# Kernel optimization log

Measured on AMD Instinct MI355X. Metric: run time of the kernel, lower is better.

The kernel has to match this reference:

```python
import jax, jax.numpy as jnp
import numpy as np

B, S, D, H, DK = 2, 2048, 1024, 16, 64
NEG = -1000000000.0


def setup_inputs() -> dict:
    key = jax.random.key(0)
    ks = jax.random.split(key, 7)
    scale = 1.0 / np.sqrt(D)
    return {
        "pos_encode_toks": jax.random.normal(ks[0], (B, S, D), dtype=jnp.float32),
        "Wq": jax.random.uniform(ks[1], (D, D), minval=-scale, maxval=scale, dtype=jnp.float32),
        "bq": jax.random.uniform(ks[2], (D,), minval=-scale, maxval=scale, dtype=jnp.float32),
        "Wk": jax.random.uniform(ks[3], (D, D), minval=-scale, maxval=scale, dtype=jnp.float32),
        "bk": jax.random.uniform(ks[4], (D,), minval=-scale, maxval=scale, dtype=jnp.float32),
        "W0": jax.random.uniform(ks[5], (D, D), minval=-scale, maxval=scale, dtype=jnp.float32),
        "b0": jax.random.uniform(ks[6], (D,), minval=-scale, maxval=scale, dtype=jnp.float32),
    }


def reference(pos_encode_toks, Wq, bq, Wk, bk, W0, b0):
    x = pos_encode_toks
    b, s, d = x.shape
    # NOTE: the original module computes V with Wq (a bug in the source) -- replicated here.
    q = (x @ Wq + bq).reshape(b, s, H, DK).transpose(0, 2, 1, 3)  # [B,H,S,DK]
    k = (x @ Wk + bk).reshape(b, s, H, DK).transpose(0, 2, 1, 3)
    v = q  # V = Wq(x), same projection as Q
    scores = jnp.einsum("bhqd,bhkd->bhqk", q, k) / np.sqrt(DK)
    causal = jnp.tril(jnp.ones((s, s), dtype=bool))
    scores = jnp.where(causal, scores, NEG)
    att_pat = jax.nn.softmax(scores, axis=-1)
    att = jnp.einsum("bhqk,bhkd->bhqd", att_pat, v)
    att = att.transpose(0, 2, 1, 3).reshape(b, s, d)
    return att @ W0 + b0
```

## Files before the change

### kernel.cpp

```cpp
#include <hip/hip_runtime.h>
#include <cstdint>
#include <cstddef>


#define AS1 __attribute__((address_space(1)))
#define AS3 __attribute__((address_space(3)))

typedef unsigned short u16;
typedef __attribute__((ext_vector_type(8))) short bf16x8;
typedef __attribute__((ext_vector_type(4))) float f32x4;

__device__ __forceinline__ u16 f2bf(float f) {
  uint32_t u = __builtin_bit_cast(uint32_t, f);
  u += 0x7fffu + ((u >> 16) & 1u);
  return (u16)(u >> 16);
}

__device__ __forceinline__ void gload16(const void* g, void* l) {
  __builtin_amdgcn_global_load_lds((const AS1 uint32_t*)(uintptr_t)g,
                                   (AS3 uint32_t*)(uintptr_t)l, 16, 0, 0);
}

__global__ __launch_bounds__(256) void cvt_x_kernel(const float* __restrict__ x,
                                                    u16* __restrict__ xb) {
  const int stride = gridDim.x * blockDim.x;
  int i = blockIdx.x * blockDim.x + threadIdx.x;
  const float4* x4 = (const float4*)x;
  ushort4* o4 = (ushort4*)xb;
  for (; i < 1048576; i += stride) {
    float4 v = x4[i];
    ushort4 o;
    o.x = f2bf(v.x); o.y = f2bf(v.y); o.z = f2bf(v.z); o.w = f2bf(v.w);
    o4[i] = o;
  }
}

__global__ __launch_bounds__(256) void transpose_w_kernel(
    const float* __restrict__ Wq, const float* __restrict__ Wk,
    const float* __restrict__ W0, u16* __restrict__ wqT,
    u16* __restrict__ wkT, u16* __restrict__ w0T) {
  const float* src; u16* dst;
  if (blockIdx.z == 0)      { src = Wq; dst = wqT; }
  else if (blockIdx.z == 1) { src = Wk; dst = wkT; }
  else                      { src = W0; dst = w0T; }
  __shared__ u16 T[64][65];
  const int k0 = blockIdx.y * 64, n0 = blockIdx.x * 64;
  const int c = threadIdx.x & 63, r0 = threadIdx.x >> 6;
#pragma unroll
  for (int i = 0; i < 16; ++i) {
    int r = i * 4 + r0;
    T[r][c] = f2bf(src[(size_t)(k0 + r) * 1024 + n0 + c]);
  }
  __syncthreads();
#pragma unroll
  for (int i = 0; i < 16; ++i) {
    int r = i * 4 + r0;
    dst[(size_t)(n0 + r) * 1024 + k0 + c] = T[c][r];
  }
}

__global__ __launch_bounds__(256) void transpose_q_kernel(const u16* __restrict__ q,
                                                          u16* __restrict__ qT) {
  const int bh = blockIdx.y;
  const int s0 = blockIdx.x * 64;
  const u16* src = q + (size_t)bh * 2048 * 64;
  u16* dst = qT + (size_t)bh * 64 * 2048;
  __shared__ u16 T[64][65];
  const int c = threadIdx.x & 63, r0 = threadIdx.x >> 6;
#pragma unroll
  for (int i = 0; i < 16; ++i) {
    int r = i * 4 + r0;
    T[r][c] = src[(size_t)(s0 + r) * 64 + c];
  }
  __syncthreads();
#pragma unroll
  for (int i = 0; i < 16; ++i) {
    int r = i * 4 + r0;
    dst[(size_t)r * 2048 + s0 + c] = T[c][r];
  }
}

template <int EPI>
__global__ __launch_bounds__(256) void gemm_kernel(
    const u16* __restrict__ A, const u16* __restrict__ BT,
    const float* __restrict__ bias, u16* __restrict__ Ob,
    float* __restrict__ Of) {
  __shared__ __align__(16) u16 As[64][64];
  __shared__ __align__(16) u16 Bs[128][64];
  const int tid = threadIdx.x, wid = tid >> 6, lane = tid & 63;
  const int l15 = lane & 15, lg = lane >> 4;
  const int bid = blockIdx.y * gridDim.x + blockIdx.x;
  const int swb = (bid & 7) * 64 + (bid >> 3);
  const int m0 = (((swb >> 6) * 8) + ((swb >> 3) & 7)) * 64;
  const int n0 = (swb & 7) * 128;
  const int wr = (wid >> 1) * 32, wc = (wid & 1) * 64;
  const int srow = lane >> 3;
  const int gz = (((lane & 7) ^ srow) * 8);

  f32x4 acc[2][4] = {};

  for (int k0 = 0; k0 < 1024; k0 += 64) {
#pragma unroll
    for (int i = 0; i < 2; ++i) {
      int chunk = wid * 2 + i;
      gload16(&A[(size_t)(m0 + chunk * 8 + srow) * 1024 + k0 + gz], &As[chunk * 8][0]);
    }
#pragma unroll
    for (int i = 0; i < 4; ++i) {
      int chunk = wid * 4 + i;
      gload16(&BT[(size_t)(n0 + chunk * 8 + srow) * 1024 + k0 + gz], &Bs[chunk * 8][0]);
    }
    __syncthreads();
#pragma unroll
    for (int kf = 0; kf < 2; ++kf) {
      const int cg = ((kf * 4 + lg) ^ (lane & 7)) * 8;
      bf16x8 af[2], bfr[4];
#pragma unroll
      for (int m = 0; m < 2; ++m)
        af[m] = *(const bf16x8*)&As[wr + m * 16 + l15][cg];
#pragma unroll
      for (int n = 0; n < 4; ++n)
        bfr[n] = *(const bf16x8*)&Bs[wc + n * 16 + l15][cg];
#pragma unroll
      for (int m = 0; m < 2; ++m)
#pragma unroll
        for (int n = 0; n < 4; ++n)
          acc[m][n] = __builtin_amdgcn_mfma_f32_16x16x32_bf16(af[m], bfr[n], acc[m][n], 0, 0, 0);
    }
    __syncthreads();
  }

  float bv[4];
#pragma unroll
  for (int n = 0; n < 4; ++n) bv[n] = bias[n0 + wc + n * 16 + l15];
#pragma unroll
  for (int m = 0; m < 2; ++m) {
#pragma unroll
    for (int r = 0; r < 4; ++r) {
      const int gm = m0 + wr + m * 16 + lg * 4 + r;
#pragma unroll
      for (int n = 0; n < 4; ++n) {
        const int gn = n0 + wc + n * 16 + l15;
        float v = acc[m][n][r] + bv[n];
        if constexpr (EPI == 2) {
          Of[(size_t)gm * 1024 + gn] = v;
        } else {
          const int b = gm >> 11, s = gm & 2047;
          const int h = gn >> 6, dk = gn & 63;
          Ob[(((size_t)(b * 16 + h)) * 2048 + s) * 64 + dk] = f2bf(v);
        }
      }
    }
  }
}

__global__ __launch_bounds__(256) void attn_kernel(const u16* __restrict__ Q,
                                                   const u16* __restrict__ K,
                                                   const u16* __restrict__ QT,
                                                   u16* __restrict__ ATT) {
  __shared__ __align__(16) u16 Ks[64][64];
  __shared__ __align__(16) u16 Vs[64][64];
  __shared__ __align__(16) u16 Ps[4][16][64];
  const int tid = threadIdx.x, wid = tid >> 6, lane = tid & 63;
  const int l15 = lane & 15, lg = lane >> 4;
  const int bid = blockIdx.y * 16 + blockIdx.x;
  const int swb = (bid & 7) * 64 + (bid >> 3);
  const int bh = (swb >> 6) * 4 + ((swb >> 4) & 3);
  const int qx = swb & 15;
  const size_t base = (size_t)bh * 2048 * 64;
  const int bb = bh >> 4, hh = bh & 15;
  const int srow = lane >> 3;
  const int gz = (((lane & 7) ^ srow) * 8);

  for (int half = 0; half < 2; ++half) {
    const int qt = half ? (31 - qx) : qx;
    const int q0 = qt * 64;
    const int wrow = q0 + wid * 16;

    bf16x8 qf[2];
#pragma unroll
    for (int kf = 0; kf < 2; ++kf)
      qf[kf] = *(const bf16x8*)&Q[base + (size_t)(wrow + l15) * 64 + kf * 32 + lg * 8];

    f32x4 o[4] = {};
    float mx[4], sm[4];
#pragma unroll
    for (int r = 0; r < 4; ++r) { mx[r] = -3e38f; sm[r] = 0.f; }

    for (int t = 0; t <= qt; ++t) {
      const int kv0 = t * 64;
#pragma unroll
      for (int i = 0; i < 2; ++i) {
        int chunk = wid * 2 + i;
        gload16(&K[base + (size_t)(kv0 + chunk * 8 + srow) * 64 + gz], &Ks[chunk * 8][0]);
        gload16(&QT[base + (size_t)(chunk * 8 + srow) * 2048 + kv0 + gz], &Vs[chunk * 8][0]);
      }
      __syncthreads();

      f32x4 sc[4] = {};
#pragma unroll
      for (int kf = 0; kf < 2; ++kf) {
        const int cg = ((kf * 4 + lg) ^ (lane & 7)) * 8;
        bf16x8 kb[4];
#pragma unroll
        for (int n = 0; n < 4; ++n)
          kb[n] = *(const bf16x8*)&Ks[n * 16 + l15][cg];
        __builtin_amdgcn_s_setprio(1);
#pragma unroll
        for (int n = 0; n < 4; ++n)
          sc[n] = __builtin_amdgcn_mfma_f32_16x16x32_bf16(qf[kf], kb[n], sc[n], 0, 0, 0);
        __builtin_amdgcn_s_setprio(0);
      }

      const bool maskt = (t == qt);
      float pr[4][4], rmax[4];
#pragma unroll
      for (int r = 0; r < 4; ++r) rmax[r] = -3e38f;
#pragma unroll
      for (int n = 0; n < 4; ++n)
#pragma unroll
        for (int r = 0; r < 4; ++r) {
          float v = sc[n][r] * 0.125f;
          if (maskt && (n * 16 + l15 > wid * 16 + lg * 4 + r)) v = -1e30f;
          pr[n][r] = v;
          rmax[r] = fmaxf(rmax[r], v);
        }
#pragma unroll
      for (int r = 0; r < 4; ++r)
#pragma unroll
        for (int d = 1; d < 16; d <<= 1)
          rmax[r] = fmaxf(rmax[r], __shfl_xor(rmax[r], d));

      float alpha[4];
#pragma unroll
      for (int r = 0; r < 4; ++r) {
        float mnew = fmaxf(mx[r], rmax[r]);
        alpha[r] = __expf(mx[r] - mnew);
        mx[r] = mnew;
        float rs = 0.f;
#pragma unroll
        for (int n = 0; n < 4; ++n) {
          float p = __expf(pr[n][r] - mnew);
          pr[n][r] = p;
          rs += p;
        }
        sm[r] = sm[r] * alpha[r] + rs;
      }
#pragma unroll
      for (int n = 0; n < 4; ++n)
#pragma unroll
        for (int r = 0; r < 4; ++r) o[n][r] *= alpha[r];

#pragma unroll
      for (int n = 0; n < 4; ++n)
#pragma unroll
        for (int r = 0; r < 4; ++r) {
          const int prow = lg * 4 + r;
          const int pcol = (n * 16 + l15) ^ ((prow & 7) << 3);
          Ps[wid][prow][pcol] = f2bf(pr[n][r]);
        }
      asm volatile("s_waitcnt lgkmcnt(0)" ::: "memory");

#pragma unroll
      for (int kf = 0; kf < 2; ++kf) {
        const int cg = ((kf * 4 + lg) ^ (lane & 7)) * 8;
        bf16x8 pa = *(const bf16x8*)&Ps[wid][l15][cg];
        bf16x8 vb[4];
#pragma unroll
        for (int n = 0; n < 4; ++n)
          vb[n] = *(const bf16x8*)&Vs[n * 16 + l15][cg];
        __builtin_amdgcn_s_setprio(1);
#pragma unroll
        for (int n = 0; n < 4; ++n)
          o[n] = __builtin_amdgcn_mfma_f32_16x16x32_bf16(pa, vb[n], o[n], 0, 0, 0);
        __builtin_amdgcn_s_setprio(0);
      }
      __syncthreads();
    }

#pragma unroll
    for (int r = 0; r < 4; ++r)
#pragma unroll
      for (int d = 1; d < 16; d <<= 1) sm[r] += __shfl_xor(sm[r], d);

#pragma unroll
    for (int r = 0; r < 4; ++r) {
      const float inv = 1.0f / sm[r];
      const int s = wrow + lg * 4 + r;
#pragma unroll
      for (int n = 0; n < 4; ++n)
        ATT[((size_t)(bb * 2048 + s)) * 1024 + hh * 64 + n * 16 + l15] =
            f2bf(o[n][r] * inv);
    }
  }
}

extern "C" void kernel_launch(void* const* d_in, const int* in_sizes, int n_in,
                              void* d_out, int out_size, void* d_ws, size_t ws_size,
                              hipStream_t stream) {
  const float* x  = (const float*)d_in[0];
  const float* Wq = (const float*)d_in[1];
  const float* bq = (const float*)d_in[2];
  const float* Wk = (const float*)d_in[3];
  const float* bk = (const float*)d_in[4];
  const float* W0 = (const float*)d_in[5];
  const float* b0 = (const float*)d_in[6];
  float* out = (float*)d_out;

  char* ws = (char*)d_ws;
  u16* xb  = (u16*)(ws + 0);
  u16* wqT = (u16*)(ws + 8388608);
  u16* wkT = (u16*)(ws + 10485760);
  u16* w0T = (u16*)(ws + 12582912);
  u16* q   = (u16*)(ws + 14680064);
  u16* k   = (u16*)(ws + 23068672);
  u16* qT  = (u16*)(ws + 31457280);
  u16* att = (u16*)(ws + 39845888);

  cvt_x_kernel<<<dim3(1024), dim3(256), 0, stream>>>(x, xb);
  transpose_w_kernel<<<dim3(16, 16, 3), dim3(256), 0, stream>>>(Wq, Wk, W0, wqT, wkT, w0T);
  gemm_kernel<0><<<dim3(64, 8), dim3(256), 0, stream>>>(xb, wqT, bq, q, nullptr);
  gemm_kernel<0><<<dim3(64, 8), dim3(256), 0, stream>>>(xb, wkT, bk, k, nullptr);
  transpose_q_kernel<<<dim3(32, 32), dim3(256), 0, stream>>>(q, qT);
  attn_kernel<<<dim3(16, 32), dim3(256), 0, stream>>>(q, k, qT, att);
  gemm_kernel<2><<<dim3(64, 8), dim3(256), 0, stream>>>(att, w0T, b0, nullptr, out);
}
```

Baseline: 200.0 us.

## Fuse Q/K projections, enlarge GEMM tiles, double-buffer attention with lazy rescaling

The Q and K projection GEMMs are merged into one launch over the concatenated, already contiguous Wq/Wk transposes, with per-column bias and output selection. The GEMM moves to 128x128 tiles with 512 threads. The attention kernel now gives each block a single query tile, longest first, and double-buffers K/V loads in shared memory so the next tile's loads overlap compute. Softmax uses exp2 with the scale folded in, and rescales the running max only when it grows by more than 8. This adds LDS use and register pressure per block, and the larger GEMM tiles give fewer blocks for the output projection.

```diff
diff --git a/kernel.cpp b/kernel.cpp
--- a/kernel.cpp
+++ b/kernel.cpp
@@ -1,4 +1,5 @@
 #include <hip/hip_runtime.h>
+#include <hip/hip_bf16.h>
 #include <cstdint>
 #include <cstddef>
 
@@ -80,218 +81,242 @@
   }
 }
 
-template <int EPI>
-__global__ __launch_bounds__(256) void gemm_kernel(
+template <int EPI, int NTILES>
+__global__ __launch_bounds__(512, 4) void gemm_kernel(
     const u16* __restrict__ A, const u16* __restrict__ BT,
-    const float* __restrict__ bias, u16* __restrict__ Ob,
-    float* __restrict__ Of) {
-  __shared__ __align__(16) u16 As[64][64];
+    const float* __restrict__ bias0, const float* __restrict__ bias1,
+    u16* __restrict__ Oq, u16* __restrict__ Ok, float* __restrict__ Of) {
+  __shared__ __align__(16) u16 As[128][64];
   __shared__ __align__(16) u16 Bs[128][64];
   const int tid = threadIdx.x, wid = tid >> 6, lane = tid & 63;
   const int l15 = lane & 15, lg = lane >> 4;
-  const int bid = blockIdx.y * gridDim.x + blockIdx.x;
-  const int swb = (bid & 7) * 64 + (bid >> 3);
-  const int m0 = (((swb >> 6) * 8) + ((swb >> 3) & 7)) * 64;
-  const int n0 = (swb & 7) * 128;
-  const int wr = (wid >> 1) * 32, wc = (wid & 1) * 64;
+  constexpr int NH = NTILES / 2;
+  const int bid = blockIdx.x;
+  const int c = bid & 7, l = bid >> 3;
+  const int m0 = ((c >> 1) * 8 + l / NH) * 128;
+  const int n0 = ((c & 1) * NH + l % NH) * 128;
+  const int wrow = (wid >> 2) * 64, wcol = (wid & 3) * 32;
   const int srow = lane >> 3;
-  const int gz = (((lane & 7) ^ srow) * 8);
-
-  f32x4 acc[2][4] = {};
+  const int gz = ((lane & 7) ^ srow) * 8;
+
+  f32x4 acc[4][2] = {};
 
   for (int k0 = 0; k0 < 1024; k0 += 64) {
 #pragma unroll
     for (int i = 0; i < 2; ++i) {
-      int chunk = wid * 2 + i;
-      gload16(&A[(size_t)(m0 + chunk * 8 + srow) * 1024 + k0 + gz], &As[chunk * 8][0]);
-    }
-#pragma unroll
-    for (int i = 0; i < 4; ++i) {
-      int chunk = wid * 4 + i;
-      gload16(&BT[(size_t)(n0 + chunk * 8 + srow) * 1024 + k0 + gz], &Bs[chunk * 8][0]);
+      int ch = wid * 2 + i;
+      gload16(&A[(size_t)(m0 + ch * 8 + srow) * 1024 + k0 + gz], &As[ch * 8][0]);
+      gload16(&BT[(size_t)(n0 + ch * 8 + srow) * 1024 + k0 + gz], &Bs[ch * 8][0]);
     }
     __syncthreads();
 #pragma unroll
     for (int kf = 0; kf < 2; ++kf) {
       const int cg = ((kf * 4 + lg) ^ (lane & 7)) * 8;
-      bf16x8 af[2], bfr[4];
-#pragma unroll
-      for (int m = 0; m < 2; ++m)
-        af[m] = *(const bf16x8*)&As[wr + m * 16 + l15][cg];
-#pragma unroll
-      for (int n = 0; n < 4; ++n)
-        bfr[n] = *(const bf16x8*)&Bs[wc + n * 16 + l15][cg];
-#pragma unroll
-      for (int m = 0; m < 2; ++m)
-#pragma unroll
-        for (int n = 0; n < 4; ++n)
+      bf16x8 af[4], bfr[2];
+#pragma unroll
+      for (int m = 0; m < 4; ++m)
+        af[m] = *(const bf16x8*)&As[wrow + m * 16 + l15][cg];
+#pragma unroll
+      for (int n = 0; n < 2; ++n)
+        bfr[n] = *(const bf16x8*)&Bs[wcol + n * 16 + l15][cg];
+#pragma unroll
+      for (int m = 0; m < 4; ++m)
+#pragma unroll
+        for (int n = 0; n < 2; ++n)
           acc[m][n] = __builtin_amdgcn_mfma_f32_16x16x32_bf16(af[m], bfr[n], acc[m][n], 0, 0, 0);
     }
     __syncthreads();
   }
 
-  float bv[4];
-#pragma unroll
-  for (int n = 0; n < 4; ++n) bv[n] = bias[n0 + wc + n * 16 + l15];
-#pragma unroll
-  for (int m = 0; m < 2; ++m) {
+  float bv[2];
+#pragma unroll
+  for (int n = 0; n < 2; ++n) {
+    const int gn = n0 + wcol + n * 16 + l15;
+    if constexpr (EPI == 0)
+      bv[n] = (gn < 1024) ? bias0[gn] : bias1[gn - 1024];
+    else
+      bv[n] = bias0[gn];
+  }
+#pragma unroll
+  for (int m = 0; m < 4; ++m) {
 #pragma unroll
     for (int r = 0; r < 4; ++r) {
-      const int gm = m0 + wr + m * 16 + lg * 4 + r;
-#pragma unroll
-      for (int n = 0; n < 4; ++n) {
-        const int gn = n0 + wc + n * 16 + l15;
+      const int gm = m0 + wrow + m * 16 + lg * 4 + r;
+#pragma unroll
+      for (int n = 0; n < 2; ++n) {
+        const int gn = n0 + wcol + n * 16 + l15;
         float v = acc[m][n][r] + bv[n];
         if constexpr (EPI == 2) {
           Of[(size_t)gm * 1024 + gn] = v;
         } else {
+          u16* dst = (gn < 1024) ? Oq : Ok;
+          const int gg = gn & 1023;
           const int b = gm >> 11, s = gm & 2047;
-          const int h = gn >> 6, dk = gn & 63;
-          Ob[(((size_t)(b * 16 + h)) * 2048 + s) * 64 + dk] = f2bf(v);
+          const int h = gg >> 6, dk = gg & 63;
+          dst[(((size_t)(b * 16 + h)) * 2048 + s) * 64 + dk] = f2bf(v);
         }
       }
     }
   }
 }
 
-__global__ __launch_bounds__(256) void attn_kernel(const u16* __restrict__ Q,
-                                                   const u16* __restrict__ K,
-                                                   const u16* __restrict__ QT,
-                                                   u16* __restrict__ ATT) {
-  __shared__ __align__(16) u16 Ks[64][64];
-  __shared__ __align__(16) u16 Vs[64][64];
+__global__ __launch_bounds__(256, 4) void attn_kernel(const u16* __restrict__ Q,
+                                                      const u16* __restrict__ K,
+                                                      const u16* __restrict__ QT,
+                                                      u16* __restrict__ ATT) {
+  __shared__ __align__(16) u16 Ks[2][64][64];
+  __shared__ __align__(16) u16 Vs[2][64][64];
   __shared__ __align__(16) u16 Ps[4][16][64];
   const int tid = threadIdx.x, wid = tid >> 6, lane = tid & 63;
   const int l15 = lane & 15, lg = lane >> 4;
-  const int bid = blockIdx.y * 16 + blockIdx.x;
-  const int swb = (bid & 7) * 64 + (bid >> 3);
-  const int bh = (swb >> 6) * 4 + ((swb >> 4) & 3);
-  const int qx = swb & 15;
+  const int bid = blockIdx.x;
+  const int bh = bid & 31;
+  const int qt = 31 - (bid >> 5);
   const size_t base = (size_t)bh * 2048 * 64;
   const int bb = bh >> 4, hh = bh & 15;
   const int srow = lane >> 3;
-  const int gz = (((lane & 7) ^ srow) * 8);
-
-  for (int half = 0; half < 2; ++half) {
-    const int qt = half ? (31 - qx) : qx;
-    const int q0 = qt * 64;
-    const int wrow = q0 + wid * 16;
-
-    bf16x8 qf[2];
-#pragma unroll
-    for (int kf = 0; kf < 2; ++kf)
-      qf[kf] = *(const bf16x8*)&Q[base + (size_t)(wrow + l15) * 64 + kf * 32 + lg * 8];
-
-    f32x4 o[4] = {};
-    float mx[4], sm[4];
-#pragma unroll
-    for (int r = 0; r < 4; ++r) { mx[r] = -3e38f; sm[r] = 0.f; }
-
-    for (int t = 0; t <= qt; ++t) {
-      const int kv0 = t * 64;
+  const int gz = ((lane & 7) ^ srow) * 8;
+  const float SCALE2 = 0.18033688011112042f;
+
+  const int q0 = qt * 64;
+  const int wrow = q0 + wid * 16;
+
+  bf16x8 qf[2];
+#pragma unroll
+  for (int kf = 0; kf < 2; ++kf)
+    qf[kf] = *(const bf16x8*)&Q[base + (size_t)(wrow + l15) * 64 + kf * 32 + lg * 8];
+
+  f32x4 o[4] = {};
+  float mx[4], sm[4];
+#pragma unroll
+  for (int r = 0; r < 4; ++r) { mx[r] = -3e38f; sm[r] = 0.f; }
+
+#pragma unroll
+  for (int i = 0; i < 2; ++i) {
+    int ch = wid * 2 + i;
+    gload16(&K[base + (size_t)(ch * 8 + srow) * 64 + gz], &Ks[0][ch * 8][0]);
+    gload16(&QT[base + (size_t)(ch * 8 + srow) * 2048 + gz], &Vs[0][ch * 8][0]);
+  }
+  __syncthreads();
+
+  for (int t = 0; t <= qt; ++t) {
+    const int cur = t & 1;
+    if (t < qt) {
+      const int kv1 = (t + 1) * 64;
 #pragma unroll
       for (int i = 0; i < 2; ++i) {
-        int chunk = wid * 2 + i;
-        gload16(&K[base + (size_t)(kv0 + chunk * 8 + srow) * 64 + gz], &Ks[chunk * 8][0]);
-        gload16(&QT[base + (size_t)(chunk * 8 + srow) * 2048 + kv0 + gz], &Vs[chunk * 8][0]);
-      }
-      __syncthreads();
-
-      f32x4 sc[4] = {};
-#pragma unroll
-      for (int kf = 0; kf < 2; ++kf) {
-        const int cg = ((kf * 4 + lg) ^ (lane & 7)) * 8;
-        bf16x8 kb[4];
-#pragma unroll
-        for (int n = 0; n < 4; ++n)
-          kb[n] = *(const bf16x8*)&Ks[n * 16 + l15][cg];
-        __builtin_amdgcn_s_setprio(1);
-#pragma unroll
-        for (int n = 0; n < 4; ++n)
-          sc[n] = __builtin_amdgcn_mfma_f32_16x16x32_bf16(qf[kf], kb[n], sc[n], 0, 0, 0);
-        __builtin_amdgcn_s_setprio(0);
-      }
-
-      const bool maskt = (t == qt);
-      float pr[4][4], rmax[4];
-#pragma unroll
-      for (int r = 0; r < 4; ++r) rmax[r] = -3e38f;
+        int ch = wid * 2 + i;
+        gload16(&K[base + (size_t)(kv1 + ch * 8 + srow) * 64 + gz], &Ks[cur ^ 1][ch * 8][0]);
+        gload16(&QT[base + (size_t)(ch * 8 + srow) * 2048 + kv1 + gz], &Vs[cur ^ 1][ch * 8][0]);
+      }
+    }
+
+    f32x4 sc[4] = {};
+#pragma unroll
+    for (int kf = 0; kf < 2; ++kf) {
+      const int cg = ((kf * 4 + lg) ^ (lane & 7)) * 8;
+      bf16x8 kb[4];
 #pragma unroll
       for (int n = 0; n < 4; ++n)
-#pragma unroll
-        for (int r = 0; r < 4; ++r) {
-          float v = sc[n][r] * 0.125f;
-          if (maskt && (n * 16 + l15 > wid * 16 + lg * 4 + r)) v = -1e30f;
-          pr[n][r] = v;
-          rmax[r] = fmaxf(rmax[r], v);
-        }
-#pragma unroll
-      for (int r = 0; r < 4; ++r)
-#pragma unroll
-        for (int d = 1; d < 16; d <<= 1)
-          rmax[r] = fmaxf(rmax[r], __shfl_xor(rmax[r], d));
-
-      float alpha[4];
+        kb[n] = *(const bf16x8*)&Ks[cur][n * 16 + l15][cg];
+      __builtin_amdgcn_s_setprio(1);
+#pragma unroll
+      for (int n = 0; n < 4; ++n)
+        sc[n] = __builtin_amdgcn_mfma_f32_16x16x32_bf16(qf[kf], kb[n], sc[n], 0, 0, 0);
+      __builtin_amdgcn_s_setprio(0);
+    }
+
+    const bool maskt = (t == qt);
+    float pr[4][4], rmax[4];
+#pragma unroll
+    for (int n = 0; n < 4; ++n)
 #pragma unroll
       for (int r = 0; r < 4; ++r) {
-        float mnew = fmaxf(mx[r], rmax[r]);
-        alpha[r] = __expf(mx[r] - mnew);
+        float v = sc[n][r] * SCALE2;
+        if (maskt && (n * 16 + l15 > wid * 16 + lg * 4 + r)) v = -1e30f;
+        pr[n][r] = v;
+      }
+#pragma unroll
+    for (int r = 0; r < 4; ++r) {
+      rmax[r] = fmaxf(fmaxf(pr[0][r], pr[1][r]), fmaxf(pr[2][r], pr[3][r]));
+#pragma unroll
+      for (int d = 1; d < 16; d <<= 1)
+        rmax[r] = fmaxf(rmax[r], __shfl_xor(rmax[r], d));
+    }
+
+    bool grow = false;
+#pragma unroll
+    for (int r = 0; r < 4; ++r) grow |= (rmax[r] > mx[r] + 8.0f);
+    if (__any(grow)) {
+#pragma unroll
+      for (int r = 0; r < 4; ++r) {
+        const float mnew = fmaxf(mx[r], rmax[r]);
+        const float alpha = exp2f(mx[r] - mnew);
         mx[r] = mnew;
-        float rs = 0.f;
-#pragma unroll
-        for (int n = 0; n < 4; ++n) {
-          float p = __expf(pr[n][r] - mnew);
-          pr[n][r] = p;
-          rs += p;
-        }
-        sm[r] = sm[r] * alpha[r] + rs;
-      }
+        sm[r] *= alpha;
+#pragma unroll
+        for (int n = 0; n < 4; ++n) o[n][r] *= alpha;
+      }
+    }
+#pragma unroll
+    for (int r = 0; r < 4; ++r) {
+      float rs = 0.f;
+#pragma unroll
+      for (int n = 0; n < 4; ++n) {
+        const float p = exp2f(pr[n][r] - mx[r]);
+        pr[n][r] = p;
+        rs += p;
+      }
+      sm[r] += rs;
+    }
+
+#pragma unroll
+    for (int r = 0; r < 4; ++r) {
+      const int prow = lg * 4 + r;
+      const int sw = (prow & 7) << 3;
+      __hip_bfloat162 c01 = __float22bfloat162_rn(make_float2(pr[0][r], pr[1][r]));
+      __hip_bfloat162 c23 = __float22bfloat162_rn(make_float2(pr[2][r], pr[3][r]));
+      u16* pp = &Ps[wid][prow][0];
+      pp[(l15)      ^ sw] = __builtin_bit_cast(u16, c01.x);
+      pp[(16 + l15) ^ sw] = __builtin_bit_cast(u16, c01.y);
+      pp[(32 + l15) ^ sw] = __builtin_bit_cast(u16, c23.x);
+      pp[(48 + l15) ^ sw] = __builtin_bit_cast(u16, c23.y);
+    }
+    asm volatile("s_waitcnt lgkmcnt(0)" ::: "memory");
+
+#pragma unroll
+    for (int kf = 0; kf < 2; ++kf) {
+      const int cg = ((kf * 4 + lg) ^ (lane & 7)) * 8;
+      bf16x8 pa = *(const bf16x8*)&Ps[wid][l15][cg];
+      bf16x8 vb[4];
 #pragma unroll
       for (int n = 0; n < 4; ++n)
-#pragma unroll
-        for (int r = 0; r < 4; ++r) o[n][r] *= alpha[r];
-
+        vb[n] = *(const bf16x8*)&Vs[cur][n * 16 + l15][cg];
+      __builtin_amdgcn_s_setprio(1);
 #pragma unroll
       for (int n = 0; n < 4; ++n)
-#pragma unroll
-        for (int r = 0; r < 4; ++r) {
-          const int prow = lg * 4 + r;
-          const int pcol = (n * 16 + l15) ^ ((prow & 7) << 3);
-          Ps[wid][prow][pcol] = f2bf(pr[n][r]);
-        }
-      asm volatile("s_waitcnt lgkmcnt(0)" ::: "memory");
-
-#pragma unroll
-      for (int kf = 0; kf < 2; ++kf) {
-        const int cg = ((kf * 4 + lg) ^ (lane & 7)) * 8;
-        bf16x8 pa = *(const bf16x8*)&Ps[wid][l15][cg];
-        bf16x8 vb[4];
-#pragma unroll
-        for (int n = 0; n < 4; ++n)
-          vb[n] = *(const bf16x8*)&Vs[n * 16 + l15][cg];
-        __builtin_amdgcn_s_setprio(1);
-#pragma unroll
-        for (int n = 0; n < 4; ++n)
-          o[n] = __builtin_amdgcn_mfma_f32_16x16x32_bf16(pa, vb[n], o[n], 0, 0, 0);
-        __builtin_amdgcn_s_setprio(0);
-      }
-      __syncthreads();
-    }
-
-#pragma unroll
-    for (int r = 0; r < 4; ++r)
-#pragma unroll
-      for (int d = 1; d < 16; d <<= 1) sm[r] += __shfl_xor(sm[r], d);
-
-#pragma unroll
-    for (int r = 0; r < 4; ++r) {
-      const float inv = 1.0f / sm[r];
-      const int s = wrow + lg * 4 + r;
-#pragma unroll
-      for (int n = 0; n < 4; ++n)
-        ATT[((size_t)(bb * 2048 + s)) * 1024 + hh * 64 + n * 16 + l15] =
-            f2bf(o[n][r] * inv);
-    }
+        o[n] = __builtin_amdgcn_mfma_f32_16x16x32_bf16(pa, vb[n], o[n], 0, 0, 0);
+      __builtin_amdgcn_s_setprio(0);
+    }
+    __syncthreads();
+  }
+
+#pragma unroll
+  for (int r = 0; r < 4; ++r)
+#pragma unroll
+    for (int d = 1; d < 16; d <<= 1) sm[r] += __shfl_xor(sm[r], d);
+
+#pragma unroll
+  for (int r = 0; r < 4; ++r) {
+    const float inv = 1.0f / sm[r];
+    const int s = wrow + lg * 4 + r;
+    __hip_bfloat162 c01 = __float22bfloat162_rn(make_float2(o[0][r] * inv, o[1][r] * inv));
+    __hip_bfloat162 c23 = __float22bfloat162_rn(make_float2(o[2][r] * inv, o[3][r] * inv));
+    u16* dst = &ATT[((size_t)(bb * 2048 + s)) * 1024 + hh * 64 + l15];
+    dst[0]  = __builtin_bit_cast(u16, c01.x);
+    dst[16] = __builtin_bit_cast(u16, c01.y);
+    dst[32] = __builtin_bit_cast(u16, c23.x);
+    dst[48] = __builtin_bit_cast(u16, c23.y);
   }
 }
 
@@ -319,9 +344,8 @@
 
   cvt_x_kernel<<<dim3(1024), dim3(256), 0, stream>>>(x, xb);
   transpose_w_kernel<<<dim3(16, 16, 3), dim3(256), 0, stream>>>(Wq, Wk, W0, wqT, wkT, w0T);
-  gemm_kernel<0><<<dim3(64, 8), dim3(256), 0, stream>>>(xb, wqT, bq, q, nullptr);
-  gemm_kernel<0><<<dim3(64, 8), dim3(256), 0, stream>>>(xb, wkT, bk, k, nullptr);
+  gemm_kernel<0, 16><<<dim3(512), dim3(512), 0, stream>>>(xb, wqT, bq, bk, q, k, nullptr);
   transpose_q_kernel<<<dim3(32, 32), dim3(256), 0, stream>>>(q, qT);
-  attn_kernel<<<dim3(16, 32), dim3(256), 0, stream>>>(q, k, qT, att);
-  gemm_kernel<2><<<dim3(64, 8), dim3(256), 0, stream>>>(att, w0T, b0, nullptr, out);
-}
+  attn_kernel<<<dim3(1024), dim3(256), 0, stream>>>(q, k, qT, att);
+  gemm_kernel<2, 8><<<dim3(256), dim3(512), 0, stream>>>(att, w0T, b0, nullptr, nullptr, nullptr, out);
+}
```

Result: faster. 183.8 us (-8.1%).
